# Kernel optimization log

Measured on AMD Instinct MI355X. Metric: run time of the kernel, lower is better.

## Reference

```python
import jax, jax.numpy as jnp
import numpy as np


def setup_inputs() -> dict:
    key = jax.random.key(0)
    ks = jax.random.split(key, 6)
    B, O, L, D, D2 = 32, 1, 2048, 1024, 512
    query = jax.random.normal(ks[0], (B, O, D), dtype=jnp.float32)
    context = jax.random.normal(ks[1], (B, L, D), dtype=jnp.float32)
    W_in = jax.random.normal(ks[2], (D, D), dtype=jnp.float32) * (1.0 / np.sqrt(D))
    W_out = jax.random.normal(ks[3], (D2, 2 * D), dtype=jnp.float32) * (1.0 / np.sqrt(2 * D))
    ae = jax.random.uniform(ks[4], (B, 1, 1), dtype=jnp.float32)
    ab = jax.random.uniform(ks[5], (B, 1, 1), dtype=jnp.float32)
    return {"query": query, "context": context, "W_in": W_in, "W_out": W_out, "ae": ae, "ab": ab}


def reference(query, context, W_in, W_out, ae, ab):
    B, O, D = query.shape  # O == 1 (required by the broadcast in mix)
    L = context.shape[1]
    # linear_in (no bias): q @ W_in^T
    q = jnp.einsum('bod,ed->boe', query, W_in)  # [B,1,D]
    # attention scores + softmax over key dimension
    scores = jnp.einsum('bod,bld->bol', q, context)  # [B,1,L]
    attn = jax.nn.softmax(scores, axis=-1)  # [B,1,L]
    # mix: weights broadcast against context^T -> [B,D,L]
    mix = attn * jnp.transpose(context, (0, 2, 1))
    # temporal decay bias: delta_t = [L-1, ..., 0]
    delta_t = jnp.arange(L - 1, -1, -1, dtype=jnp.float32).reshape(1, 1, L)
    bt = jnp.exp(-ab * delta_t)  # [B,1,L]
    term_2 = jax.nn.relu(ae * mix * bt)  # [B,D,L]
    mixed = jnp.sum(term_2 + mix, axis=-1)[:, None, :]  # [B,1,D]
    combined = jnp.concatenate([mixed, q], axis=2)  # [B,1,2D]
    out = jnp.tanh(jnp.einsum('boc,ec->boe', combined, W_out))  # [B,1,D2]
    return (out, attn)
```

## Files before the change

### kernel.cpp

```cpp
#include <hip/hip_runtime.h>
#include <hip/hip_bf16.h>

#define NB 32
#define NL 2048
#define ND 1024
#define ND2 512

typedef unsigned short ushort_t;

__device__ __forceinline__ float bf2f(unsigned int u16) {
    return __uint_as_float(u16 << 16);
}
__device__ __forceinline__ void cvt8(uint4 v, float* f) {
    f[0] = bf2f(v.x & 0xffffu); f[1] = bf2f(v.x >> 16);
    f[2] = bf2f(v.y & 0xffffu); f[3] = bf2f(v.y >> 16);
    f[4] = bf2f(v.z & 0xffffu); f[5] = bf2f(v.z >> 16);
    f[6] = bf2f(v.w & 0xffffu); f[7] = bf2f(v.w >> 16);
}
__device__ __forceinline__ void load8(const void* p, size_t idx, int isf32, float* f) {
    if (isf32) {
        const float4* fp = (const float4*)((const float*)p + idx);
        float4 a = fp[0], b = fp[1];
        f[0]=a.x; f[1]=a.y; f[2]=a.z; f[3]=a.w;
        f[4]=b.x; f[5]=b.y; f[6]=b.z; f[7]=b.w;
    } else {
        uint4 v = *(const uint4*)((const ushort_t*)p + idx);
        cvt8(v, f);
    }
}
__device__ __forceinline__ float load1(const void* p, int idx, int isf32) {
    return isf32 ? ((const float*)p)[idx] : bf2f(((const ushort_t*)p)[idx]);
}
__device__ __forceinline__ void store1(void* p, size_t idx, float v, int isf32) {
    if (isf32) ((float*)p)[idx] = v;
    else ((__hip_bfloat16*)p)[idx] = __float2bfloat16(v);
}
__device__ __forceinline__ float waveReduceSum(float v) {
    for (int off = 32; off > 0; off >>= 1) v += __shfl_down(v, off, 64);
    return v;
}

__global__ void k_detect(const ushort_t* __restrict__ ctx, int* __restrict__ flag) {
    __shared__ int found;
    if (threadIdx.x == 0) found = 0;
    __syncthreads();
    int cnt = 0;
    for (int i = threadIdx.x; i < 16384; i += 256) {
        unsigned e = (ctx[i] >> 7) & 0xFFu;
        if (e == 0xFFu) cnt++;
    }
    if (cnt) atomicOr(&found, 1);
    __syncthreads();
    if (threadIdx.x == 0) *flag = found;
}

__global__ __launch_bounds__(256) void k_qproj(const void* __restrict__ query,
                                               const void* __restrict__ W_in,
                                               float* __restrict__ q,
                                               const int* __restrict__ flag) {
    int isf32 = *flag;
    int wave = blockIdx.x * 4 + (threadIdx.x >> 6);
    int lane = threadIdx.x & 63;
    int b = wave >> 10;
    int e = wave & 1023;
    size_t qb = (size_t)b * ND + lane * 16;
    size_t wb = (size_t)e * ND + lane * 16;
    float qa[8], qc[8], wa[8], wc[8];
    load8(query, qb, isf32, qa); load8(query, qb + 8, isf32, qc);
    load8(W_in, wb, isf32, wa);  load8(W_in, wb + 8, isf32, wc);
    float s = 0.f;
    for (int i = 0; i < 8; i++) s += qa[i] * wa[i] + qc[i] * wc[i];
    s = waveReduceSum(s);
    if (lane == 0) q[b * ND + e] = s;
}

__global__ __launch_bounds__(256) void k_scores(const float* __restrict__ q,
                                                const void* __restrict__ ctx,
                                                float* __restrict__ scores,
                                                const int* __restrict__ flag) {
    int isf32 = *flag;
    int wave = blockIdx.x * 4 + (threadIdx.x >> 6);
    int lane = threadIdx.x & 63;
    int b = wave >> 9;
    int lg = wave & 511;
    int l0 = lg * 4;
    const float4* qp = (const float4*)(q + b * ND) + lane * 4;
    float4 q0 = qp[0], q1 = qp[1], q2 = qp[2], q3 = qp[3];
    for (int j = 0; j < 4; j++) {
        int l = l0 + j;
        size_t base = ((size_t)b * NL + l) * ND + lane * 16;
        float ca[8], cb[8];
        load8(ctx, base, isf32, ca); load8(ctx, base + 8, isf32, cb);
        float s = q0.x*ca[0]+q0.y*ca[1]+q0.z*ca[2]+q0.w*ca[3]
                + q1.x*ca[4]+q1.y*ca[5]+q1.z*ca[6]+q1.w*ca[7]
                + q2.x*cb[0]+q2.y*cb[1]+q2.z*cb[2]+q2.w*cb[3]
                + q3.x*cb[4]+q3.y*cb[5]+q3.z*cb[6]+q3.w*cb[7];
        s = waveReduceSum(s);
        if (lane == 0) scores[b * NL + l] = s;
    }
}

__global__ __launch_bounds__(256) void k_softmax(float* __restrict__ scores,
                                                 const void* __restrict__ ae,
                                                 const void* __restrict__ ab,
                                                 float* __restrict__ c2,
                                                 void* __restrict__ d_out,
                                                 const int* __restrict__ flag) {
    int isf32 = *flag;
    int b = blockIdx.x;
    int tid = threadIdx.x;
    __shared__ float red[256];
    float s[8];
    for (int k = 0; k < 8; k++) s[k] = scores[b * NL + tid + k * 256];
    float m = s[0];
    for (int k = 1; k < 8; k++) m = fmaxf(m, s[k]);
    red[tid] = m; __syncthreads();
    for (int step = 128; step > 0; step >>= 1) {
        if (tid < step) red[tid] = fmaxf(red[tid], red[tid + step]);
        __syncthreads();
    }
    m = red[0]; __syncthreads();
    float e[8], loc = 0.f;
    for (int k = 0; k < 8; k++) { e[k] = expf(s[k] - m); loc += e[k]; }
    red[tid] = loc; __syncthreads();
    for (int step = 128; step > 0; step >>= 1) {
        if (tid < step) red[tid] += red[tid + step];
        __syncthreads();
    }
    float inv = 1.f / red[0];
    float aev = load1(ae, b, isf32), abv = load1(ab, b, isf32);
    for (int k = 0; k < 8; k++) {
        int l = tid + k * 256;
        float a = e[k] * inv;
        scores[b * NL + l] = a;
        c2[b * NL + l] = aev * a * expf(-abv * (float)(NL - 1 - l));
        store1(d_out, (size_t)NB * ND2 + b * NL + l, a, isf32);
    }
}

#define LCHUNK 128
__global__ __launch_bounds__(256) void k_mix(const void* __restrict__ ctx,
                                             const float* __restrict__ attn,
                                             const float* __restrict__ c2,
                                             float* __restrict__ partials,
                                             const int* __restrict__ flag) {
    int isf32 = *flag;
    int b = blockIdx.x >> 4;
    int chunk = blockIdx.x & 15;
    int l0 = chunk * LCHUNK;
    int tid = threadIdx.x;
    __shared__ float sc1[LCHUNK], sc2[LCHUNK];
    __shared__ float comb[128 * 8];
    if (tid < LCHUNK) sc1[tid] = attn[b * NL + l0 + tid];
    else sc2[tid - LCHUNK] = c2[b * NL + l0 + tid - LCHUNK];
    __syncthreads();
    int half = tid >> 7;
    int dgrp = tid & 127;
    int d0 = dgrp * 8;
    float acc[8];
    for (int j = 0; j < 8; j++) acc[j] = 0.f;
    for (int l = half; l < LCHUNK; l += 2) {
        float f[8];
        load8(ctx, ((size_t)b * NL + l0 + l) * ND + d0, isf32, f);
        float a = sc1[l], k2 = sc2[l];
        for (int j = 0; j < 8; j++) acc[j] += a * f[j] + k2 * fmaxf(f[j], 0.f);
    }
    if (half == 1) {
        for (int j = 0; j < 8; j++) comb[dgrp * 8 + j] = acc[j];
    }
    __syncthreads();
    if (half == 0) {
        float* outp = partials + ((size_t)(b * 16 + chunk)) * ND + d0;
        for (int j = 0; j < 8; j++) outp[j] = acc[j] + comb[dgrp * 8 + j];
    }
}

__global__ __launch_bounds__(256) void k_reduce(const float* __restrict__ partials,
                                               float* __restrict__ mixed) {
    int idx = blockIdx.x * 256 + threadIdx.x;
    int b = idx >> 10, d = idx & 1023;
    float s = 0.f;
    for (int c = 0; c < 16; c++) s += partials[((size_t)(b * 16 + c)) * ND + d];
    mixed[idx] = s;
}

__global__ __launch_bounds__(256) void k_out(const float* __restrict__ mixed,
                                             const float* __restrict__ q,
                                             const void* __restrict__ W_out,
                                             void* __restrict__ d_out,
                                             const int* __restrict__ flag) {
    int isf32 = *flag;
    int wave = blockIdx.x * 4 + (threadIdx.x >> 6);
    int lane = threadIdx.x & 63;
    int b = wave >> 9;
    int e = wave & 511;
    int c0 = lane * 32;
    const float* src = (lane < 32) ? (mixed + b * ND + c0) : (q + b * ND + c0 - ND);
    float s = 0.f;
    for (int t = 0; t < 4; t++) {
        float w[8];
        load8(W_out, (size_t)e * 2 * ND + c0 + t * 8, isf32, w);
        const float4* sp = (const float4*)(src + t * 8);
        float4 s0 = sp[0], s1 = sp[1];
        s += w[0]*s0.x + w[1]*s0.y + w[2]*s0.z + w[3]*s0.w
           + w[4]*s1.x + w[5]*s1.y + w[6]*s1.z + w[7]*s1.w;
    }
    s = waveReduceSum(s);
    if (lane == 0) store1(d_out, (size_t)b * ND2 + e, tanhf(s), isf32);
}

extern "C" void kernel_launch(void* const* d_in, const int* in_sizes, int n_in,
                              void* d_out, int out_size, void* d_ws, size_t ws_size,
                              hipStream_t stream) {
    const void* query = d_in[0];
    const void* ctx   = d_in[1];
    const void* W_in  = d_in[2];
    const void* W_out = d_in[3];
    const void* ae    = d_in[4];
    const void* ab    = d_in[5];

    float* ws       = (float*)d_ws;
    float* q        = ws;
    float* scores   = ws + 32768;
    float* c2       = ws + 98304;
    float* partials = ws + 163840;
    float* mixed    = ws + 688128;
    int*   flag     = (int*)(ws + 720896);

    k_detect <<<   1, 256, 0, stream>>>((const ushort_t*)ctx, flag);
    k_qproj  <<<8192, 256, 0, stream>>>(query, W_in, q, flag);
    k_scores <<<4096, 256, 0, stream>>>(q, ctx, scores, flag);
    k_softmax<<<  32, 256, 0, stream>>>(scores, ae, ab, c2, d_out, flag);
    k_mix    <<< 512, 256, 0, stream>>>(ctx, scores, c2, partials, flag);
    k_reduce <<< 128, 256, 0, stream>>>(partials, mixed);
    k_out    <<<4096, 256, 0, stream>>>(mixed, q, W_out, d_out, flag);
}
```

Measured before the change: 482.4 us.

## Fuse scores, softmax and mix into single-pass online-softmax flash kernel

```diff
diff --git a/kernel.cpp b/kernel.cpp
--- a/kernel.cpp
+++ b/kernel.cpp
@@ -1,237 +1,202 @@
 #include <hip/hip_runtime.h>
 #include <hip/hip_bf16.h>
+#include <math.h>
 
 #define NB 32
 #define NL 2048
 #define ND 1024
 #define ND2 512
-
-typedef unsigned short ushort_t;
-
-__device__ __forceinline__ float bf2f(unsigned int u16) {
-    return __uint_as_float(u16 << 16);
-}
-__device__ __forceinline__ void cvt8(uint4 v, float* f) {
-    f[0] = bf2f(v.x & 0xffffu); f[1] = bf2f(v.x >> 16);
-    f[2] = bf2f(v.y & 0xffffu); f[3] = bf2f(v.y >> 16);
-    f[4] = bf2f(v.z & 0xffffu); f[5] = bf2f(v.z >> 16);
-    f[6] = bf2f(v.w & 0xffffu); f[7] = bf2f(v.w >> 16);
-}
-__device__ __forceinline__ void load8(const void* p, size_t idx, int isf32, float* f) {
-    if (isf32) {
-        const float4* fp = (const float4*)((const float*)p + idx);
-        float4 a = fp[0], b = fp[1];
-        f[0]=a.x; f[1]=a.y; f[2]=a.z; f[3]=a.w;
-        f[4]=b.x; f[5]=b.y; f[6]=b.z; f[7]=b.w;
-    } else {
-        uint4 v = *(const uint4*)((const ushort_t*)p + idx);
-        cvt8(v, f);
-    }
-}
-__device__ __forceinline__ float load1(const void* p, int idx, int isf32) {
-    return isf32 ? ((const float*)p)[idx] : bf2f(((const ushort_t*)p)[idx]);
-}
-__device__ __forceinline__ void store1(void* p, size_t idx, float v, int isf32) {
-    if (isf32) ((float*)p)[idx] = v;
-    else ((__hip_bfloat16*)p)[idx] = __float2bfloat16(v);
+#define CH 32
+#define ROWS (NL / CH)
+#define RPW (ROWS / 4)
+
+__device__ __forceinline__ float waveReduceSumAll(float v) {
+    for (int off = 32; off > 0; off >>= 1) v += __shfl_xor(v, off, 64);
+    return v;
 }
 __device__ __forceinline__ float waveReduceSum(float v) {
     for (int off = 32; off > 0; off >>= 1) v += __shfl_down(v, off, 64);
     return v;
 }
 
-__global__ void k_detect(const ushort_t* __restrict__ ctx, int* __restrict__ flag) {
-    __shared__ int found;
-    if (threadIdx.x == 0) found = 0;
-    __syncthreads();
-    int cnt = 0;
-    for (int i = threadIdx.x; i < 16384; i += 256) {
-        unsigned e = (ctx[i] >> 7) & 0xFFu;
-        if (e == 0xFFu) cnt++;
-    }
-    if (cnt) atomicOr(&found, 1);
-    __syncthreads();
-    if (threadIdx.x == 0) *flag = found;
-}
-
-__global__ __launch_bounds__(256) void k_qproj(const void* __restrict__ query,
-                                               const void* __restrict__ W_in,
-                                               float* __restrict__ q,
-                                               const int* __restrict__ flag) {
-    int isf32 = *flag;
+__global__ __launch_bounds__(256) void k_qproj(const float* __restrict__ query,
+                                               const float* __restrict__ W_in,
+                                               float* __restrict__ q) {
     int wave = blockIdx.x * 4 + (threadIdx.x >> 6);
     int lane = threadIdx.x & 63;
     int b = wave >> 10;
     int e = wave & 1023;
-    size_t qb = (size_t)b * ND + lane * 16;
-    size_t wb = (size_t)e * ND + lane * 16;
-    float qa[8], qc[8], wa[8], wc[8];
-    load8(query, qb, isf32, qa); load8(query, qb + 8, isf32, qc);
-    load8(W_in, wb, isf32, wa);  load8(W_in, wb + 8, isf32, wc);
+    const float4* qr = (const float4*)(query + (size_t)b * ND) + lane * 4;
+    const float4* wr = (const float4*)(W_in + (size_t)e * ND) + lane * 4;
     float s = 0.f;
-    for (int i = 0; i < 8; i++) s += qa[i] * wa[i] + qc[i] * wc[i];
+#pragma unroll
+    for (int t = 0; t < 4; t++) {
+        float4 a = qr[t], w = wr[t];
+        s += a.x * w.x + a.y * w.y + a.z * w.z + a.w * w.w;
+    }
     s = waveReduceSum(s);
     if (lane == 0) q[b * ND + e] = s;
 }
 
-__global__ __launch_bounds__(256) void k_scores(const float* __restrict__ q,
-                                                const void* __restrict__ ctx,
-                                                float* __restrict__ scores,
-                                                const int* __restrict__ flag) {
-    int isf32 = *flag;
-    int wave = blockIdx.x * 4 + (threadIdx.x >> 6);
+__global__ __launch_bounds__(256) void k_flash(const float* __restrict__ q,
+                                               const float* __restrict__ ctx,
+                                               const float* __restrict__ ae,
+                                               const float* __restrict__ ab,
+                                               float* __restrict__ scores,
+                                               float* __restrict__ pm,
+                                               float* __restrict__ pZ,
+                                               float* __restrict__ pacc) {
+    int b = blockIdx.x >> 5;
+    int chunk = blockIdx.x & 31;
+    int wave = threadIdx.x >> 6;
     int lane = threadIdx.x & 63;
-    int b = wave >> 9;
-    int lg = wave & 511;
-    int l0 = lg * 4;
-    const float4* qp = (const float4*)(q + b * ND) + lane * 4;
+
+    const float4* qp = (const float4*)(q + (size_t)b * ND) + lane * 4;
     float4 q0 = qp[0], q1 = qp[1], q2 = qp[2], q3 = qp[3];
-    for (int j = 0; j < 4; j++) {
-        int l = l0 + j;
-        size_t base = ((size_t)b * NL + l) * ND + lane * 16;
-        float ca[8], cb[8];
-        load8(ctx, base, isf32, ca); load8(ctx, base + 8, isf32, cb);
-        float s = q0.x*ca[0]+q0.y*ca[1]+q0.z*ca[2]+q0.w*ca[3]
-                + q1.x*ca[4]+q1.y*ca[5]+q1.z*ca[6]+q1.w*ca[7]
-                + q2.x*cb[0]+q2.y*cb[1]+q2.z*cb[2]+q2.w*cb[3]
-                + q3.x*cb[4]+q3.y*cb[5]+q3.z*cb[6]+q3.w*cb[7];
-        s = waveReduceSum(s);
+    float aev = ae[b], abv = ab[b];
+
+    float m = -INFINITY, Z = 0.f;
+    float acc[16];
+#pragma unroll
+    for (int j = 0; j < 16; j++) acc[j] = 0.f;
+
+    int l0 = chunk * ROWS + wave * RPW;
+    for (int i = 0; i < RPW; i++) {
+        int l = l0 + i;
+        const float4* cp = (const float4*)(ctx + ((size_t)b * NL + l) * ND) + lane * 4;
+        float4 c0 = cp[0], c1 = cp[1], c2 = cp[2], c3 = cp[3];
+        float s = c0.x*q0.x + c0.y*q0.y + c0.z*q0.z + c0.w*q0.w
+                + c1.x*q1.x + c1.y*q1.y + c1.z*q1.z + c1.w*q1.w
+                + c2.x*q2.x + c2.y*q2.y + c2.z*q2.z + c2.w*q2.w
+                + c3.x*q3.x + c3.y*q3.y + c3.z*q3.z + c3.w*q3.w;
+        s = waveReduceSumAll(s);
         if (lane == 0) scores[b * NL + l] = s;
-    }
-}
-
-__global__ __launch_bounds__(256) void k_softmax(float* __restrict__ scores,
-                                                 const void* __restrict__ ae,
-                                                 const void* __restrict__ ab,
-                                                 float* __restrict__ c2,
-                                                 void* __restrict__ d_out,
-                                                 const int* __restrict__ flag) {
-    int isf32 = *flag;
+
+        float bt = __expf(-abv * (float)(NL - 1 - l));
+        if (s > m) {
+            float sc = __expf(m - s);
+            m = s;
+            Z *= sc;
+#pragma unroll
+            for (int j = 0; j < 16; j++) acc[j] *= sc;
+        }
+        float p = __expf(s - m);
+        float k2 = p * aev * bt;
+        Z += p;
+        float c[16] = {c0.x,c0.y,c0.z,c0.w, c1.x,c1.y,c1.z,c1.w,
+                       c2.x,c2.y,c2.z,c2.w, c3.x,c3.y,c3.z,c3.w};
+#pragma unroll
+        for (int j = 0; j < 16; j++)
+            acc[j] += p * c[j] + k2 * fmaxf(c[j], 0.f);
+    }
+
+    __shared__ float sacc[4 * ND];
+    __shared__ float sm[4], sZ[4];
+#pragma unroll
+    for (int j = 0; j < 16; j++) sacc[wave * ND + lane * 16 + j] = acc[j];
+    if (lane == 0) { sm[wave] = m; sZ[wave] = Z; }
+    __syncthreads();
+
+    int tid = threadIdx.x;
+    float m0 = sm[0], m1 = sm[1], m2 = sm[2], m3 = sm[3];
+    float mb = fmaxf(fmaxf(m0, m1), fmaxf(m2, m3));
+    float e0 = __expf(m0 - mb), e1 = __expf(m1 - mb),
+          e2 = __expf(m2 - mb), e3 = __expf(m3 - mb);
+    int d = tid * 4;
+    float4 v;
+    v.x = e0*sacc[0*ND+d+0] + e1*sacc[1*ND+d+0] + e2*sacc[2*ND+d+0] + e3*sacc[3*ND+d+0];
+    v.y = e0*sacc[0*ND+d+1] + e1*sacc[1*ND+d+1] + e2*sacc[2*ND+d+1] + e3*sacc[3*ND+d+1];
+    v.z = e0*sacc[0*ND+d+2] + e1*sacc[1*ND+d+2] + e2*sacc[2*ND+d+2] + e3*sacc[3*ND+d+2];
+    v.w = e0*sacc[0*ND+d+3] + e1*sacc[1*ND+d+3] + e2*sacc[2*ND+d+3] + e3*sacc[3*ND+d+3];
+    *(float4*)(pacc + ((size_t)(b * CH + chunk)) * ND + d) = v;
+    if (tid == 0) {
+        pm[b * CH + chunk] = mb;
+        pZ[b * CH + chunk] = e0*sZ[0] + e1*sZ[1] + e2*sZ[2] + e3*sZ[3];
+    }
+}
+
+__global__ __launch_bounds__(256) void k_merge(const float* __restrict__ pm,
+                                               const float* __restrict__ pZ,
+                                               const float* __restrict__ pacc,
+                                               const float* __restrict__ scores,
+                                               float* __restrict__ mixed,
+                                               float* __restrict__ attn_out) {
     int b = blockIdx.x;
     int tid = threadIdx.x;
-    __shared__ float red[256];
-    float s[8];
-    for (int k = 0; k < 8; k++) s[k] = scores[b * NL + tid + k * 256];
-    float m = s[0];
-    for (int k = 1; k < 8; k++) m = fmaxf(m, s[k]);
-    red[tid] = m; __syncthreads();
-    for (int step = 128; step > 0; step >>= 1) {
-        if (tid < step) red[tid] = fmaxf(red[tid], red[tid + step]);
-        __syncthreads();
-    }
-    m = red[0]; __syncthreads();
-    float e[8], loc = 0.f;
-    for (int k = 0; k < 8; k++) { e[k] = expf(s[k] - m); loc += e[k]; }
-    red[tid] = loc; __syncthreads();
-    for (int step = 128; step > 0; step >>= 1) {
-        if (tid < step) red[tid] += red[tid + step];
-        __syncthreads();
-    }
-    float inv = 1.f / red[0];
-    float aev = load1(ae, b, isf32), abv = load1(ab, b, isf32);
-    for (int k = 0; k < 8; k++) {
-        int l = tid + k * 256;
-        float a = e[k] * inv;
-        scores[b * NL + l] = a;
-        c2[b * NL + l] = aev * a * expf(-abv * (float)(NL - 1 - l));
-        store1(d_out, (size_t)NB * ND2 + b * NL + l, a, isf32);
-    }
-}
-
-#define LCHUNK 128
-__global__ __launch_bounds__(256) void k_mix(const void* __restrict__ ctx,
-                                             const float* __restrict__ attn,
-                                             const float* __restrict__ c2,
-                                             float* __restrict__ partials,
-                                             const int* __restrict__ flag) {
-    int isf32 = *flag;
-    int b = blockIdx.x >> 4;
-    int chunk = blockIdx.x & 15;
-    int l0 = chunk * LCHUNK;
-    int tid = threadIdx.x;
-    __shared__ float sc1[LCHUNK], sc2[LCHUNK];
-    __shared__ float comb[128 * 8];
-    if (tid < LCHUNK) sc1[tid] = attn[b * NL + l0 + tid];
-    else sc2[tid - LCHUNK] = c2[b * NL + l0 + tid - LCHUNK];
+    __shared__ float ew[CH];
+    __shared__ float smg, sinvZ;
+    if (tid == 0) {
+        float mg = -INFINITY;
+        for (int i = 0; i < CH; i++) mg = fmaxf(mg, pm[b * CH + i]);
+        float Zg = 0.f;
+        for (int i = 0; i < CH; i++) Zg += __expf(pm[b * CH + i] - mg) * pZ[b * CH + i];
+        smg = mg; sinvZ = 1.f / Zg;
+    }
     __syncthreads();
-    int half = tid >> 7;
-    int dgrp = tid & 127;
-    int d0 = dgrp * 8;
-    float acc[8];
-    for (int j = 0; j < 8; j++) acc[j] = 0.f;
-    for (int l = half; l < LCHUNK; l += 2) {
-        float f[8];
-        load8(ctx, ((size_t)b * NL + l0 + l) * ND + d0, isf32, f);
-        float a = sc1[l], k2 = sc2[l];
-        for (int j = 0; j < 8; j++) acc[j] += a * f[j] + k2 * fmaxf(f[j], 0.f);
-    }
-    if (half == 1) {
-        for (int j = 0; j < 8; j++) comb[dgrp * 8 + j] = acc[j];
-    }
+    float mg = smg, invZ = sinvZ;
+    if (tid < CH) ew[tid] = __expf(pm[b * CH + tid] - mg);
     __syncthreads();
-    if (half == 0) {
-        float* outp = partials + ((size_t)(b * 16 + chunk)) * ND + d0;
-        for (int j = 0; j < 8; j++) outp[j] = acc[j] + comb[dgrp * 8 + j];
-    }
-}
-
-__global__ __launch_bounds__(256) void k_reduce(const float* __restrict__ partials,
-                                               float* __restrict__ mixed) {
-    int idx = blockIdx.x * 256 + threadIdx.x;
-    int b = idx >> 10, d = idx & 1023;
-    float s = 0.f;
-    for (int c = 0; c < 16; c++) s += partials[((size_t)(b * 16 + c)) * ND + d];
-    mixed[idx] = s;
+
+    int d = tid * 4;
+    float4 accv = {0.f, 0.f, 0.f, 0.f};
+    for (int i = 0; i < CH; i++) {
+        float4 pv = *(const float4*)(pacc + ((size_t)(b * CH + i)) * ND + d);
+        float e = ew[i];
+        accv.x += e * pv.x; accv.y += e * pv.y;
+        accv.z += e * pv.z; accv.w += e * pv.w;
+    }
+    accv.x *= invZ; accv.y *= invZ; accv.z *= invZ; accv.w *= invZ;
+    *(float4*)(mixed + (size_t)b * ND + d) = accv;
+
+    for (int l = tid; l < NL; l += 256)
+        attn_out[b * NL + l] = __expf(scores[b * NL + l] - mg) * invZ;
 }
 
 __global__ __launch_bounds__(256) void k_out(const float* __restrict__ mixed,
                                              const float* __restrict__ q,
-                                             const void* __restrict__ W_out,
-                                             void* __restrict__ d_out,
-                                             const int* __restrict__ flag) {
-    int isf32 = *flag;
+                                             const float* __restrict__ W_out,
+                                             float* __restrict__ out) {
     int wave = blockIdx.x * 4 + (threadIdx.x >> 6);
     int lane = threadIdx.x & 63;
     int b = wave >> 9;
     int e = wave & 511;
     int c0 = lane * 32;
-    const float* src = (lane < 32) ? (mixed + b * ND + c0) : (q + b * ND + c0 - ND);
+    const float* src = (lane < 32) ? (mixed + (size_t)b * ND + c0)
+                                   : (q + (size_t)b * ND + c0 - ND);
+    const float4* wr = (const float4*)(W_out + (size_t)e * 2 * ND + c0);
+    const float4* sp = (const float4*)src;
     float s = 0.f;
-    for (int t = 0; t < 4; t++) {
-        float w[8];
-        load8(W_out, (size_t)e * 2 * ND + c0 + t * 8, isf32, w);
-        const float4* sp = (const float4*)(src + t * 8);
-        float4 s0 = sp[0], s1 = sp[1];
-        s += w[0]*s0.x + w[1]*s0.y + w[2]*s0.z + w[3]*s0.w
-           + w[4]*s1.x + w[5]*s1.y + w[6]*s1.z + w[7]*s1.w;
+#pragma unroll
+    for (int t = 0; t < 8; t++) {
+        float4 w = wr[t], x = sp[t];
+        s += w.x * x.x + w.y * x.y + w.z * x.z + w.w * x.w;
     }
     s = waveReduceSum(s);
-    if (lane == 0) store1(d_out, (size_t)b * ND2 + e, tanhf(s), isf32);
+    if (lane == 0) out[b * ND2 + e] = tanhf(s);
 }
 
 extern "C" void kernel_launch(void* const* d_in, const int* in_sizes, int n_in,
                               void* d_out, int out_size, void* d_ws, size_t ws_size,
                               hipStream_t stream) {
-    const void* query = d_in[0];
-    const void* ctx   = d_in[1];
-    const void* W_in  = d_in[2];
-    const void* W_out = d_in[3];
-    const void* ae    = d_in[4];
-    const void* ab    = d_in[5];
-
-    float* ws       = (float*)d_ws;
-    float* q        = ws;
-    float* scores   = ws + 32768;
-    float* c2       = ws + 98304;
-    float* partials = ws + 163840;
-    float* mixed    = ws + 688128;
-    int*   flag     = (int*)(ws + 720896);
-
-    k_detect <<<   1, 256, 0, stream>>>((const ushort_t*)ctx, flag);
-    k_qproj  <<<8192, 256, 0, stream>>>(query, W_in, q, flag);
-    k_scores <<<4096, 256, 0, stream>>>(q, ctx, scores, flag);
-    k_softmax<<<  32, 256, 0, stream>>>(scores, ae, ab, c2, d_out, flag);
-    k_mix    <<< 512, 256, 0, stream>>>(ctx, scores, c2, partials, flag);
-    k_reduce <<< 128, 256, 0, stream>>>(partials, mixed);
-    k_out    <<<4096, 256, 0, stream>>>(mixed, q, W_out, d_out, flag);
-}
+    const float* query = (const float*)d_in[0];
+    const float* ctx   = (const float*)d_in[1];
+    const float* W_in  = (const float*)d_in[2];
+    const float* W_out = (const float*)d_in[3];
+    const float* ae    = (const float*)d_in[4];
+    const float* ab    = (const float*)d_in[5];
+    float* out = (float*)d_out;
+    float* attn_out = out + (size_t)NB * ND2;
+
+    float* ws     = (float*)d_ws;
+    float* q      = ws;
+    float* scores = ws + 32768;
+    float* pm     = ws + 98304;
+    float* pZ     = ws + 99328;
+    float* pacc   = ws + 100352;
+    float* mixed  = ws + 1148928;
+
+    k_qproj<<<8192, 256, 0, stream>>>(query, W_in, q);
+    k_flash<<<NB * CH, 256, 0, stream>>>(q, ctx, ae, ab, scores, pm, pZ, pacc);
+    k_merge<<<NB, 256, 0, stream>>>(pm, pZ, pacc, scores, mixed, attn_out);
+    k_out<<<4096, 256, 0, stream>>>(mixed, q, W_out, out);
+}
```

Result: faster. 429.0 us (-11.1%).
